# Kernel optimization log

Hardware: AMD Instinct MI355X
Metric: run time of the kernel (lower is better)

Reference implementation:

```python
import jax, jax.numpy as jnp
import numpy as np

UNITS = 512


def setup_inputs() -> dict:
    key = jax.random.key(0)
    k0, k1, k2 = jax.random.split(key, 3)
    batch, timesteps, input_dim = 64, 512, 512
    inputs = jax.random.normal(k0, (batch, timesteps, input_dim), dtype=jnp.float32)
    # Keras glorot_uniform for kernel
    limit = np.sqrt(6.0 / (input_dim + 3 * UNITS))
    kernel = jax.random.uniform(k1, (input_dim, 3 * UNITS), dtype=jnp.float32,
                                minval=-limit, maxval=limit)
    # orthogonal init for recurrent kernel
    recurrent_kernel = jax.nn.initializers.orthogonal()(k2, (UNITS, 3 * UNITS), jnp.float32)
    bias = jnp.zeros((2, 3 * UNITS), dtype=jnp.float32)
    return {"inputs": inputs, "kernel": kernel,
            "recurrent_kernel": recurrent_kernel, "bias": bias}


def _gru_forward(inputs, kernel, recurrent_kernel, bias):
    units = recurrent_kernel.shape[0]
    batch = inputs.shape[0]
    input_bias, recurrent_bias = bias[0], bias[1]
    # Precompute input projections for all timesteps: [B, T, 3U]
    x_all = jnp.einsum('bti,ig->btg', inputs, kernel) + input_bias
    x_all_t = jnp.swapaxes(x_all, 0, 1)  # [T, B, 3U] for scan
    h0 = jnp.zeros((batch, units), dtype=inputs.dtype)

    def step(h, x_t):
        x_z, x_r, x_h = jnp.split(x_t, 3, axis=-1)
        rec = h @ recurrent_kernel + recurrent_bias  # [B, 3U]
        rec_z, rec_r, rec_h = jnp.split(rec, 3, axis=-1)
        z = jax.nn.sigmoid(x_z + rec_z)
        r = jax.nn.sigmoid(x_r + rec_r)
        hh = jnp.tanh(x_h + r * rec_h)
        h_new = z * h + (1.0 - z) * hh
        return h_new, h_new

    _, outs = jax.lax.scan(step, h0, x_all_t)  # outs: [T, B, U]
    return jnp.swapaxes(outs, 0, 1)  # [B, T, U] (return_sequences=True)


def reference(inputs, kernel, recurrent_kernel, bias):
    return _gru_forward(inputs, kernel, recurrent_kernel, bias)
```

## Files before the change

### kernel.cpp

```cpp
#include <hip/hip_runtime.h>
#include <hip/hip_bf16.h>


typedef float f32x4 __attribute__((ext_vector_type(4)));
typedef float f32x2 __attribute__((ext_vector_type(2)));
typedef short bf16x8 __attribute__((ext_vector_type(8)));
typedef unsigned long long u64;
typedef unsigned int u32;
typedef unsigned short u16;
typedef u32 u32x4 __attribute__((ext_vector_type(4)));

#define MFMA16(a, b, c) __builtin_amdgcn_mfma_f32_16x16x32_bf16((a), (b), (c), 0, 0, 0)

__device__ __forceinline__ float bf2f(__hip_bfloat16 v) { return __bfloat162float(v); }

__device__ __forceinline__ void split_bf(float v, short& hi, short& lo) {
    __hip_bfloat16 h = __float2bfloat16(v);
    float rem = v - __bfloat162float(h);
    __hip_bfloat16 l = __float2bfloat16(rem);
    hi = __builtin_bit_cast(short, h);
    lo = __builtin_bit_cast(short, l);
}

__device__ __forceinline__ void wg_barrier() {
    __builtin_amdgcn_sched_barrier(0);
    asm volatile("s_waitcnt lgkmcnt(0)" ::: "memory");
    __builtin_amdgcn_s_barrier();
    __builtin_amdgcn_sched_barrier(0);
}

__global__ void zero_kernel(float* p, int n) {
    int i = blockIdx.x * blockDim.x + threadIdx.x;
    int stride = gridDim.x * blockDim.x;
    for (; i < n; i += stride) p[i] = 0.f;
}

__global__ __launch_bounds__(64, 1) void pack_w_kernel(const float* __restrict__ W,
                                                       short* __restrict__ dhi,
                                                       short* __restrict__ dlo) {
    int bid = blockIdx.x;
    int lane = threadIdx.x;
    int col = (bid >> 4) * 16 + (lane & 15);
    int kbase = (bid & 15) * 32 + (lane >> 4) * 8;
    bf16x8 vh, vl;
#pragma unroll
    for (int e = 0; e < 8; e++) {
        float v = W[(kbase + e) * 1536 + col];
        short h, l;
        split_bf(v, h, l);
        vh[e] = h;
        vl[e] = l;
    }
    *(bf16x8*)(dhi + bid * 512 + lane * 8) = vh;
    *(bf16x8*)(dlo + bid * 512 + lane * 8) = vl;
}

__global__ __launch_bounds__(256, 2) void xgemm_kernel(
    const float* __restrict__ A, const short* __restrict__ wkh,
    const short* __restrict__ wkl, const float* __restrict__ bias,
    __hip_bfloat16* __restrict__ xhi, __hip_bfloat16* __restrict__ xlo, int xlo_en) {
    int rt = blockIdx.x;
    int wave = threadIdx.x >> 6, lane = threadIdx.x & 63;
    int arow = rt * 16 + (lane & 15);
    const float* abase = A + arow * 512 + (lane >> 4) * 8;

    f32x4 acc[24];
#pragma unroll
    for (int j = 0; j < 24; j++) acc[j] = (f32x4){0.f, 0.f, 0.f, 0.f};

#pragma unroll 1
    for (int kk = 0; kk < 16; kk++) {
        f32x4 a0 = *(const f32x4*)(abase + kk * 32);
        f32x4 a1 = *(const f32x4*)(abase + kk * 32 + 4);
        bf16x8 ah, al;
#pragma unroll
        for (int e = 0; e < 8; e++) {
            float v = (e < 4) ? a0[e] : a1[e - 4];
            short h, l;
            split_bf(v, h, l);
            ah[e] = h;
            al[e] = l;
        }
#pragma unroll
        for (int j = 0; j < 24; j++) {
            int frag = (wave * 24 + j) * 16 + kk;
            bf16x8 bh = *(const bf16x8*)(wkh + frag * 512 + lane * 8);
            bf16x8 bl = *(const bf16x8*)(wkl + frag * 512 + lane * 8);
            acc[j] = MFMA16(ah, bh, acc[j]);
            acc[j] = MFMA16(al, bh, acc[j]);
            acc[j] = MFMA16(ah, bl, acc[j]);
        }
    }
    int colin = lane & 15, r4 = (lane >> 4) * 4;
#pragma unroll
    for (int j = 0; j < 24; j++) {
        int colg = (wave * 24 + j) * 16 + colin;
        float bv = bias[colg];
#pragma unroll
        for (int r = 0; r < 4; r++) {
            float v = acc[j][r] + bv;
            int rowg = rt * 16 + r4 + r;
            short h, l;
            split_bf(v, h, l);
            xhi[rowg * 1536 + colg] = __builtin_bit_cast(__hip_bfloat16, h);
            if (xlo_en) xlo[rowg * 1536 + colg] = __builtin_bit_cast(__hip_bfloat16, l);
        }
    }
}

__global__ __launch_bounds__(512, 1) void scan_kernel(
    const __hip_bfloat16* __restrict__ xhi, const __hip_bfloat16* __restrict__ xlo,
    const short* __restrict__ wrh, const short* __restrict__ wrl,
    const float* __restrict__ bias, float* __restrict__ out,
    u64* hbuf2, int xlo_en) {
    const int bid = blockIdx.x;
    const int g = bid & 3;
    const int w = bid >> 2;
    const int tid = threadIdx.x;
    const int wave = tid >> 6;
    const int lane = tid & 63;

    __shared__ __align__(16) float pre[6][16][16];
    __shared__ __align__(16) __hip_bfloat16 xsh[2][2][16][104];
    __shared__ __align__(16) __hip_bfloat16 hsh[2][2][16][512];
    __shared__ float rb[96];

    if (tid < 96) rb[tid] = bias[1536 + (tid >> 5) * 512 + w * 32 + (tid & 31)];

    bf16x8 bh[16], bl[16];
    if (wave < 6) {
        int tile = (wave >> 1) * 32 + 2 * w + (wave & 1);
#pragma unroll
        for (int kk = 0; kk < 16; kk++) {
            bh[kk] = *(const bf16x8*)(wrh + (tile * 16 + kk) * 512 + lane * 8);
            bl[kk] = *(const bf16x8*)(wrl + (tile * 16 + kk) * 512 + lane * 8);
        }
#pragma unroll
        for (int kk = 0; kk < 16; kk++) {
            asm volatile("" : "+v"(bh[kk]), "+v"(bl[kk]));
        }
    } else {
        int it0 = tid - 384;
        int nch = xlo_en ? 384 : 192;
        for (int c = it0; c < nch; c += 128) {
            int plane = c / 192, rem = c % 192;
            int row_ = rem / 12, cw = rem % 12;
            const __hip_bfloat16* src = (plane ? xlo : xhi) +
                                        (size_t)((g * 16 + row_) * 512) * 1536 +
                                        (cw >> 2) * 512 + w * 32 + (cw & 3) * 8;
            *(bf16x8*)&xsh[0][plane][row_][(cw >> 2) * 32 + (cw & 3) * 8] =
                *(const bf16x8*)src;
        }
    }

    const int grow = tid & 15;
    const int q = tid >> 4;
    float h0 = 0.f, h1 = 0.f;
    const int hslot = w * 256 + (grow + 16 * (q >> 2)) * 4 + (q & 3);
    const int sA = tid * 4;
    const int sB = 2048 + tid * 4;
    const int xit = tid - 384;

    u32* hshu = (u32*)hsh;

    __syncthreads();

    for (int t = 0; t < 512; t++) {
        const int par = t & 1;
        u64 sv[8];
        {
            const u64* gb = hbuf2 + ((size_t)(((t - 1) & 1) * 4 + g)) * 4096;
            if (t == 0) {
#pragma unroll
                for (int j = 0; j < 4; j++)
                    sv[j] = __hip_atomic_load(gb + sA + j, __ATOMIC_RELAXED,
                                              __HIP_MEMORY_SCOPE_AGENT);
#pragma unroll
                for (int j = 0; j < 4; j++)
                    sv[4 + j] = __hip_atomic_load(gb + sB + j, __ATOMIC_RELAXED,
                                                  __HIP_MEMORY_SCOPE_AGENT);
            } else {
                const int expv = ((t - 1) % 3) + 1;
                const u64 expm =
                    ((u64)(expv & 1) << 32) | ((u64)((expv >> 1) & 1) << 48);
                const u64 TAGM = (1ULL << 32) | (1ULL << 48);
                long spins = 0;
                while (true) {
#pragma unroll
                    for (int j = 0; j < 4; j++)
                        sv[j] = __hip_atomic_load(gb + sA + j, __ATOMIC_RELAXED,
                                                  __HIP_MEMORY_SCOPE_AGENT);
#pragma unroll
                    for (int j = 0; j < 4; j++)
                        sv[4 + j] = __hip_atomic_load(gb + sB + j, __ATOMIC_RELAXED,
                                                      __HIP_MEMORY_SCOPE_AGENT);
                    u64 diff = 0;
#pragma unroll
                    for (int j = 0; j < 8; j++) diff |= (sv[j] ^ expm) & TAGM;
                    if (diff == 0) break;
                    if (++spins > (1L << 20)) break;
                }
            }
        }
        bf16x8 xv0, xv1, xv2;
        if (wave >= 6 && t + 1 < 512) {
            int c0 = xit, c1 = xit + 128, c2 = xit + 256;
            {
                int plane = c0 / 192, rem = c0 % 192, row_ = rem / 12, cw = rem % 12;
                xv0 = *(const bf16x8*)((plane ? xlo : xhi) +
                                       (size_t)((g * 16 + row_) * 512 + (t + 1)) * 1536 +
                                       (cw >> 2) * 512 + w * 32 + (cw & 3) * 8);
            }
            if (xlo_en || c1 < 192) {
                int plane = c1 / 192, rem = c1 % 192, row_ = rem / 12, cw = rem % 12;
                xv1 = *(const bf16x8*)((plane ? xlo : xhi) +
                                       (size_t)((g * 16 + row_) * 512 + (t + 1)) * 1536 +
                                       (cw >> 2) * 512 + w * 32 + (cw & 3) * 8);
            }
            if (xlo_en) {
                int plane = 1, rem = c2 % 192, row_ = rem / 12, cw = rem % 12;
                xv2 = *(const bf16x8*)((plane ? xlo : xhi) +
                                       (size_t)((g * 16 + row_) * 512 + (t + 1)) * 1536 +
                                       (cw >> 2) * 512 + w * 32 + (cw & 3) * 8);
            }
        }
        {
            u32* hp = hshu + par * 8192;
            u32x4 a0, a1, b0, b1;
#pragma unroll
            for (int j = 0; j < 4; j++) {
                a0[j] = (u32)sv[j];
                b0[j] = (u32)(sv[j] >> 32);
                a1[j] = (u32)sv[4 + j];
                b1[j] = (u32)(sv[4 + j] >> 32);
            }
            *(u32x4*)&hp[sA] = a0;
            *(u32x4*)&hp[sB] = a1;
            *(u32x4*)&hp[4096 + sA] = b0;
            *(u32x4*)&hp[4096 + sB] = b1;
        }
        wg_barrier();
        if (wave < 6) {
            f32x4 aa = (f32x4){0.f, 0.f, 0.f, 0.f};
            f32x4 ab = (f32x4){0.f, 0.f, 0.f, 0.f};
            f32x4 ac = (f32x4){0.f, 0.f, 0.f, 0.f};
#pragma unroll
            for (int kk = 0; kk < 16; kk++) {
                bf16x8 ah = *(const bf16x8*)&hsh[par][0][kk][lane * 8];
                bf16x8 al = *(const bf16x8*)&hsh[par][1][kk][lane * 8];
                aa = MFMA16(ah, bh[kk], aa);
                ab = MFMA16(al, bh[kk], ab);
                ac = MFMA16(ah, bl[kk], ac);
            }
            f32x4 acc = aa + ab;
            acc = acc + ac;
            *(f32x4*)&pre[wave][lane & 15][(lane >> 4) * 4] = acc;
        } else if (t + 1 < 512) {
            int npar = (t + 1) & 1;
            int c0 = xit, c1 = xit + 128, c2 = xit + 256;
            {
                int plane = c0 / 192, rem = c0 % 192, row_ = rem / 12, cw = rem % 12;
                *(bf16x8*)&xsh[npar][plane][row_][(cw >> 2) * 32 + (cw & 3) * 8] = xv0;
            }
            if (xlo_en || c1 < 192) {
                int plane = c1 / 192, rem = c1 % 192, row_ = rem / 12, cw = rem % 12;
                *(bf16x8*)&xsh[npar][plane][row_][(cw >> 2) * 32 + (cw & 3) * 8] = xv1;
            }
            if (xlo_en) {
                int plane = 1, rem = c2 % 192, row_ = rem / 12, cw = rem % 12;
                *(bf16x8*)&xsh[npar][plane][row_][(cw >> 2) * 32 + (cw & 3) * 8] = xv2;
            }
        }
        wg_barrier();
        if (tid < 256) {
            float hold[2] = {h0, h1};
            float hn[2];
#pragma unroll
            for (int j = 0; j < 2; j++) {
                int uu = 2 * q + j;
                int sl = uu >> 4, c16 = uu & 15;
                float xz = bf2f(xsh[par][0][grow][uu]);
                float xr = bf2f(xsh[par][0][grow][32 + uu]);
                float xh = bf2f(xsh[par][0][grow][64 + uu]);
                if (xlo_en) {
                    xz += bf2f(xsh[par][1][grow][uu]);
                    xr += bf2f(xsh[par][1][grow][32 + uu]);
                    xh += bf2f(xsh[par][1][grow][64 + uu]);
                }
                float rz = pre[sl][c16][grow] + rb[uu];
                float rr = pre[2 + sl][c16][grow] + rb[32 + uu];
                float rh = pre[4 + sl][c16][grow] + rb[64 + uu];
                float z = 1.f / (1.f + expf(-(xz + rz)));
                float r = 1.f / (1.f + expf(-(xr + rr)));
                float hh = tanhf(xh + r * rh);
                hn[j] = z * hold[j] + (1.f - z) * hh;
            }
            h0 = hn[0];
            h1 = hn[1];
            if (t < 511) {
                short hi0, lo0, hi1, lo1;
                split_bf(hn[0], hi0, lo0);
                split_bf(hn[1], hi1, lo1);
                const u32 tag = (u32)(t % 3) + 1;
                u32 lo0m = ((u32)(u16)lo0 & ~1u) | (tag & 1);
                u32 lo1m = ((u32)(u16)lo1 & ~1u) | ((tag >> 1) & 1);
                u64 v = (u64)(u16)hi0 | ((u64)(u16)hi1 << 16) | ((u64)lo0m << 32) |
                        ((u64)lo1m << 48);
                __hip_atomic_store(&hbuf2[((size_t)(par * 4 + g)) * 4096 + hslot], v,
                                   __ATOMIC_RELAXED, __HIP_MEMORY_SCOPE_AGENT);
            }
            *(f32x2*)&out[((size_t)(g * 16 + grow) * 512 + t) * 512 + w * 32 + 2 * q] =
                (f32x2){h0, h1};
        }
    }
}

extern "C" void kernel_launch(void* const* d_in, const int* in_sizes, int n_in,
                              void* d_out, int out_size, void* d_ws, size_t ws_size,
                              hipStream_t stream) {
    const float* inputs = (const float*)d_in[0];
    const float* wk = (const float*)d_in[1];
    const float* wr = (const float*)d_in[2];
    const float* bias = (const float*)d_in[3];
    float* out = (float*)d_out;
    char* ws = (char*)d_ws;

    const size_t SZ_W = 512UL * 1536 * 2;
    short* wk_hi = (short*)(ws);
    short* wk_lo = (short*)(ws + SZ_W);
    short* wr_hi = (short*)(ws + 2 * SZ_W);
    short* wr_lo = (short*)(ws + 3 * SZ_W);
    u64* hbuf2 = (u64*)(ws + 4 * SZ_W);
    char* xbase = ws + 4 * SZ_W + 262144;
    const size_t SZ_X = 32768UL * 1536 * 2;
    __hip_bfloat16* xhi = (__hip_bfloat16*)xbase;
    __hip_bfloat16* xlo = (__hip_bfloat16*)(xbase + SZ_X);

    size_t need_min = (size_t)(xbase - ws) + SZ_X;
    size_t need_full = need_min + SZ_X;
    if (ws_size < need_min) return;
    int xlo_en = (ws_size >= need_full) ? 1 : 0;

    zero_kernel<<<256, 256, 0, stream>>>((float*)hbuf2, 262144 / 4);
    pack_w_kernel<<<1536, 64, 0, stream>>>(wk, wk_hi, wk_lo);
    pack_w_kernel<<<1536, 64, 0, stream>>>(wr, wr_hi, wr_lo);
    xgemm_kernel<<<2048, 256, 0, stream>>>(inputs, wk_hi, wk_lo, bias, xhi, xlo, xlo_en);
    scan_kernel<<<64, 512, 0, stream>>>(xhi, xlo, wr_hi, wr_lo, bias, out, hbuf2,
                                        xlo_en);
}
```

Measured before the change: 2.521 ms.

## Retile input GEMM into row-pair by column-group blocks and move h polling to waves 4-7

The input-projection GEMM now gives each block two 16-row tiles and one third of the output columns, launched over 3072 blocks. Each loaded weight fragment is reused across both row tiles and fewer accumulators are held per wave. In the scan kernel, only the four non-MFMA waves (4-7) poll the global hidden-state buffer and copy it into LDS. The MFMA waves go straight to the barrier, and the x prefetch stores are issued after the barrier to overlap with the recurrent MFMA. This is meant to shorten the per-step critical path, at the cost of more loads per polling thread and a changed barrier pattern.

```diff
diff --git a/kernel.cpp b/kernel.cpp
--- a/kernel.cpp
+++ b/kernel.cpp
@@ -59,51 +59,70 @@
     const float* __restrict__ A, const short* __restrict__ wkh,
     const short* __restrict__ wkl, const float* __restrict__ bias,
     __hip_bfloat16* __restrict__ xhi, __hip_bfloat16* __restrict__ xlo, int xlo_en) {
-    int rt = blockIdx.x;
+    int bid = blockIdx.x;
+    int cg = bid % 3;
+    int rp = bid / 3;
     int wave = threadIdx.x >> 6, lane = threadIdx.x & 63;
-    int arow = rt * 16 + (lane & 15);
-    const float* abase = A + arow * 512 + (lane >> 4) * 8;
-
-    f32x4 acc[24];
-#pragma unroll
-    for (int j = 0; j < 24; j++) acc[j] = (f32x4){0.f, 0.f, 0.f, 0.f};
+    int arow0 = rp * 32 + (lane & 15);
+    const float* ab0 = A + (size_t)arow0 * 512 + (lane >> 4) * 8;
+    const float* ab1 = ab0 + 16 * 512;
+
+    f32x4 acc[2][8];
+#pragma unroll
+    for (int r = 0; r < 2; r++)
+#pragma unroll
+        for (int j = 0; j < 8; j++) acc[r][j] = (f32x4){0.f, 0.f, 0.f, 0.f};
 
 #pragma unroll 1
     for (int kk = 0; kk < 16; kk++) {
-        f32x4 a0 = *(const f32x4*)(abase + kk * 32);
-        f32x4 a1 = *(const f32x4*)(abase + kk * 32 + 4);
-        bf16x8 ah, al;
+        f32x4 a00 = *(const f32x4*)(ab0 + kk * 32);
+        f32x4 a01 = *(const f32x4*)(ab0 + kk * 32 + 4);
+        f32x4 a10 = *(const f32x4*)(ab1 + kk * 32);
+        f32x4 a11 = *(const f32x4*)(ab1 + kk * 32 + 4);
+        bf16x8 ah0, al0, ah1, al1;
 #pragma unroll
         for (int e = 0; e < 8; e++) {
-            float v = (e < 4) ? a0[e] : a1[e - 4];
+            float v0 = (e < 4) ? a00[e] : a01[e - 4];
+            float v1 = (e < 4) ? a10[e] : a11[e - 4];
             short h, l;
-            split_bf(v, h, l);
-            ah[e] = h;
-            al[e] = l;
-        }
-#pragma unroll
-        for (int j = 0; j < 24; j++) {
-            int frag = (wave * 24 + j) * 16 + kk;
+            split_bf(v0, h, l);
+            ah0[e] = h;
+            al0[e] = l;
+            split_bf(v1, h, l);
+            ah1[e] = h;
+            al1[e] = l;
+        }
+#pragma unroll
+        for (int j = 0; j < 8; j++) {
+            int frag = (cg * 32 + wave * 8 + j) * 16 + kk;
             bf16x8 bh = *(const bf16x8*)(wkh + frag * 512 + lane * 8);
             bf16x8 bl = *(const bf16x8*)(wkl + frag * 512 + lane * 8);
-            acc[j] = MFMA16(ah, bh, acc[j]);
-            acc[j] = MFMA16(al, bh, acc[j]);
-            acc[j] = MFMA16(ah, bl, acc[j]);
+            acc[0][j] = MFMA16(ah0, bh, acc[0][j]);
+            acc[0][j] = MFMA16(al0, bh, acc[0][j]);
+            acc[0][j] = MFMA16(ah0, bl, acc[0][j]);
+            acc[1][j] = MFMA16(ah1, bh, acc[1][j]);
+            acc[1][j] = MFMA16(al1, bh, acc[1][j]);
+            acc[1][j] = MFMA16(ah1, bl, acc[1][j]);
         }
     }
     int colin = lane & 15, r4 = (lane >> 4) * 4;
 #pragma unroll
-    for (int j = 0; j < 24; j++) {
-        int colg = (wave * 24 + j) * 16 + colin;
+    for (int j = 0; j < 8; j++) {
+        int colg = (cg * 32 + wave * 8 + j) * 16 + colin;
         float bv = bias[colg];
 #pragma unroll
-        for (int r = 0; r < 4; r++) {
-            float v = acc[j][r] + bv;
-            int rowg = rt * 16 + r4 + r;
-            short h, l;
-            split_bf(v, h, l);
-            xhi[rowg * 1536 + colg] = __builtin_bit_cast(__hip_bfloat16, h);
-            if (xlo_en) xlo[rowg * 1536 + colg] = __builtin_bit_cast(__hip_bfloat16, l);
+        for (int rt = 0; rt < 2; rt++) {
+#pragma unroll
+            for (int r = 0; r < 4; r++) {
+                float v = acc[rt][j][r] + bv;
+                int rowg = rp * 32 + rt * 16 + r4 + r;
+                short h, l;
+                split_bf(v, h, l);
+                xhi[(size_t)rowg * 1536 + colg] = __builtin_bit_cast(__hip_bfloat16, h);
+                if (xlo_en)
+                    xlo[(size_t)rowg * 1536 + colg] =
+                        __builtin_bit_cast(__hip_bfloat16, l);
+            }
         }
     }
 }
@@ -139,7 +158,8 @@
         for (int kk = 0; kk < 16; kk++) {
             asm volatile("" : "+v"(bh[kk]), "+v"(bl[kk]));
         }
-    } else {
+    }
+    if (wave >= 6) {
         int it0 = tid - 384;
         int nch = xlo_en ? 384 : 192;
         for (int c = it0; c < nch; c += 128) {
@@ -157,8 +177,7 @@
     const int q = tid >> 4;
     float h0 = 0.f, h1 = 0.f;
     const int hslot = w * 256 + (grow + 16 * (q >> 2)) * 4 + (q & 3);
-    const int sA = tid * 4;
-    const int sB = 2048 + tid * 4;
+    const int st = tid - 256;
     const int xit = tid - 384;
 
     u32* hshu = (u32*)hsh;
@@ -167,79 +186,110 @@
 
     for (int t = 0; t < 512; t++) {
         const int par = t & 1;
-        u64 sv[8];
-        {
-            const u64* gb = hbuf2 + ((size_t)(((t - 1) & 1) * 4 + g)) * 4096;
-            if (t == 0) {
-#pragma unroll
-                for (int j = 0; j < 4; j++)
-                    sv[j] = __hip_atomic_load(gb + sA + j, __ATOMIC_RELAXED,
-                                              __HIP_MEMORY_SCOPE_AGENT);
-#pragma unroll
-                for (int j = 0; j < 4; j++)
-                    sv[4 + j] = __hip_atomic_load(gb + sB + j, __ATOMIC_RELAXED,
+        if (wave >= 4) {
+            bf16x8 xv0, xv1, xv2;
+            if (wave >= 6 && t + 1 < 512) {
+                int c0 = xit, c1 = xit + 128, c2 = xit + 256;
+                {
+                    int plane = c0 / 192, rem = c0 % 192, row_ = rem / 12,
+                        cw = rem % 12;
+                    xv0 = *(const bf16x8*)((plane ? xlo : xhi) +
+                                           (size_t)((g * 16 + row_) * 512 + (t + 1)) *
+                                               1536 +
+                                           (cw >> 2) * 512 + w * 32 + (cw & 3) * 8);
+                }
+                if (xlo_en || c1 < 192) {
+                    int plane = c1 / 192, rem = c1 % 192, row_ = rem / 12,
+                        cw = rem % 12;
+                    xv1 = *(const bf16x8*)((plane ? xlo : xhi) +
+                                           (size_t)((g * 16 + row_) * 512 + (t + 1)) *
+                                               1536 +
+                                           (cw >> 2) * 512 + w * 32 + (cw & 3) * 8);
+                }
+                if (xlo_en) {
+                    int plane = 1, rem = c2 % 192, row_ = rem / 12, cw = rem % 12;
+                    xv2 = *(const bf16x8*)((plane ? xlo : xhi) +
+                                           (size_t)((g * 16 + row_) * 512 + (t + 1)) *
+                                               1536 +
+                                           (cw >> 2) * 512 + w * 32 + (cw & 3) * 8);
+                }
+            }
+            u64 sv[16];
+            {
+                const u64* gb = hbuf2 + ((size_t)(((t - 1) & 1) * 4 + g)) * 4096;
+                if (t == 0) {
+#pragma unroll
+                    for (int r = 0; r < 4; r++)
+#pragma unroll
+                        for (int j = 0; j < 4; j++)
+                            sv[r * 4 + j] =
+                                __hip_atomic_load(gb + r * 1024 + st * 4 + j,
+                                                  __ATOMIC_RELAXED,
                                                   __HIP_MEMORY_SCOPE_AGENT);
+                } else {
+                    const int expv = ((t - 1) % 3) + 1;
+                    const u64 expm =
+                        ((u64)(expv & 1) << 32) | ((u64)((expv >> 1) & 1) << 48);
+                    const u64 TAGM = (1ULL << 32) | (1ULL << 48);
+                    long spins = 0;
+                    while (true) {
+#pragma unroll
+                        for (int r = 0; r < 4; r++)
+#pragma unroll
+                            for (int j = 0; j < 4; j++)
+                                sv[r * 4 + j] =
+                                    __hip_atomic_load(gb + r * 1024 + st * 4 + j,
+                                                      __ATOMIC_RELAXED,
+                                                      __HIP_MEMORY_SCOPE_AGENT);
+                        u64 diff = 0;
+#pragma unroll
+                        for (int k = 0; k < 16; k++) diff |= (sv[k] ^ expm) & TAGM;
+                        if (diff == 0) break;
+                        if (++spins > (1L << 20)) break;
+                    }
+                }
+            }
+            {
+                u32* hp = hshu + par * 8192;
+#pragma unroll
+                for (int r = 0; r < 4; r++) {
+                    u32x4 vlo, vhi;
+#pragma unroll
+                    for (int j = 0; j < 4; j++) {
+                        vlo[j] = (u32)sv[r * 4 + j];
+                        vhi[j] = (u32)(sv[r * 4 + j] >> 32);
+                    }
+                    *(u32x4*)&hp[r * 1024 + st * 4] = vlo;
+                    *(u32x4*)&hp[4096 + r * 1024 + st * 4] = vhi;
+                }
+            }
+            if (wave >= 6 && t + 1 < 512) {
+                wg_barrier();
+                int npar = (t + 1) & 1;
+                int c0 = xit, c1 = xit + 128, c2 = xit + 256;
+                {
+                    int plane = c0 / 192, rem = c0 % 192, row_ = rem / 12,
+                        cw = rem % 12;
+                    *(bf16x8*)&xsh[npar][plane][row_][(cw >> 2) * 32 + (cw & 3) * 8] =
+                        xv0;
+                }
+                if (xlo_en || c1 < 192) {
+                    int plane = c1 / 192, rem = c1 % 192, row_ = rem / 12,
+                        cw = rem % 12;
+                    *(bf16x8*)&xsh[npar][plane][row_][(cw >> 2) * 32 + (cw & 3) * 8] =
+                        xv1;
+                }
+                if (xlo_en) {
+                    int plane = 1, rem = c2 % 192, row_ = rem / 12, cw = rem % 12;
+                    *(bf16x8*)&xsh[npar][plane][row_][(cw >> 2) * 32 + (cw & 3) * 8] =
+                        xv2;
+                }
             } else {
-                const int expv = ((t - 1) % 3) + 1;
-                const u64 expm =
-                    ((u64)(expv & 1) << 32) | ((u64)((expv >> 1) & 1) << 48);
-                const u64 TAGM = (1ULL << 32) | (1ULL << 48);
-                long spins = 0;
-                while (true) {
-#pragma unroll
-                    for (int j = 0; j < 4; j++)
-                        sv[j] = __hip_atomic_load(gb + sA + j, __ATOMIC_RELAXED,
-                                                  __HIP_MEMORY_SCOPE_AGENT);
-#pragma unroll
-                    for (int j = 0; j < 4; j++)
-                        sv[4 + j] = __hip_atomic_load(gb + sB + j, __ATOMIC_RELAXED,
-                                                      __HIP_MEMORY_SCOPE_AGENT);
-                    u64 diff = 0;
-#pragma unroll
-                    for (int j = 0; j < 8; j++) diff |= (sv[j] ^ expm) & TAGM;
-                    if (diff == 0) break;
-                    if (++spins > (1L << 20)) break;
-                }
-            }
-        }
-        bf16x8 xv0, xv1, xv2;
-        if (wave >= 6 && t + 1 < 512) {
-            int c0 = xit, c1 = xit + 128, c2 = xit + 256;
-            {
-                int plane = c0 / 192, rem = c0 % 192, row_ = rem / 12, cw = rem % 12;
-                xv0 = *(const bf16x8*)((plane ? xlo : xhi) +
-                                       (size_t)((g * 16 + row_) * 512 + (t + 1)) * 1536 +
-                                       (cw >> 2) * 512 + w * 32 + (cw & 3) * 8);
-            }
-            if (xlo_en || c1 < 192) {
-                int plane = c1 / 192, rem = c1 % 192, row_ = rem / 12, cw = rem % 12;
-                xv1 = *(const bf16x8*)((plane ? xlo : xhi) +
-                                       (size_t)((g * 16 + row_) * 512 + (t + 1)) * 1536 +
-                                       (cw >> 2) * 512 + w * 32 + (cw & 3) * 8);
-            }
-            if (xlo_en) {
-                int plane = 1, rem = c2 % 192, row_ = rem / 12, cw = rem % 12;
-                xv2 = *(const bf16x8*)((plane ? xlo : xhi) +
-                                       (size_t)((g * 16 + row_) * 512 + (t + 1)) * 1536 +
-                                       (cw >> 2) * 512 + w * 32 + (cw & 3) * 8);
-            }
-        }
-        {
-            u32* hp = hshu + par * 8192;
-            u32x4 a0, a1, b0, b1;
-#pragma unroll
-            for (int j = 0; j < 4; j++) {
-                a0[j] = (u32)sv[j];
-                b0[j] = (u32)(sv[j] >> 32);
-                a1[j] = (u32)sv[4 + j];
-                b1[j] = (u32)(sv[4 + j] >> 32);
-            }
-            *(u32x4*)&hp[sA] = a0;
-            *(u32x4*)&hp[sB] = a1;
-            *(u32x4*)&hp[4096 + sA] = b0;
-            *(u32x4*)&hp[4096 + sB] = b1;
-        }
-        wg_barrier();
+                wg_barrier();
+            }
+        } else {
+            wg_barrier();
+        }
         if (wave < 6) {
             f32x4 aa = (f32x4){0.f, 0.f, 0.f, 0.f};
             f32x4 ab = (f32x4){0.f, 0.f, 0.f, 0.f};
@@ -255,21 +305,6 @@
             f32x4 acc = aa + ab;
             acc = acc + ac;
             *(f32x4*)&pre[wave][lane & 15][(lane >> 4) * 4] = acc;
-        } else if (t + 1 < 512) {
-            int npar = (t + 1) & 1;
-            int c0 = xit, c1 = xit + 128, c2 = xit + 256;
-            {
-                int plane = c0 / 192, rem = c0 % 192, row_ = rem / 12, cw = rem % 12;
-                *(bf16x8*)&xsh[npar][plane][row_][(cw >> 2) * 32 + (cw & 3) * 8] = xv0;
-            }
-            if (xlo_en || c1 < 192) {
-                int plane = c1 / 192, rem = c1 % 192, row_ = rem / 12, cw = rem % 12;
-                *(bf16x8*)&xsh[npar][plane][row_][(cw >> 2) * 32 + (cw & 3) * 8] = xv1;
-            }
-            if (xlo_en) {
-                int plane = 1, rem = c2 % 192, row_ = rem / 12, cw = rem % 12;
-                *(bf16x8*)&xsh[npar][plane][row_][(cw >> 2) * 32 + (cw & 3) * 8] = xv2;
-            }
         }
         wg_barrier();
         if (tid < 256) {
@@ -344,7 +379,7 @@
     zero_kernel<<<256, 256, 0, stream>>>((float*)hbuf2, 262144 / 4);
     pack_w_kernel<<<1536, 64, 0, stream>>>(wk, wk_hi, wk_lo);
     pack_w_kernel<<<1536, 64, 0, stream>>>(wr, wr_hi, wr_lo);
-    xgemm_kernel<<<2048, 256, 0, stream>>>(inputs, wk_hi, wk_lo, bias, xhi, xlo, xlo_en);
+    xgemm_kernel<<<3072, 256, 0, stream>>>(inputs, wk_hi, wk_lo, bias, xhi, xlo, xlo_en);
     scan_kernel<<<64, 512, 0, stream>>>(xhi, xlo, wr_hi, wr_lo, bias, out, hbuf2,
                                         xlo_en);
 }
```

After: 2.555 ms. About the same (+1.4%).

## Retile input GEMM for weight reuse and double-buffer scan spin-wait loads

Applied to the files above, without the earlier changes.

The input projection GEMM now has each block compute a 64-row by 512-column tile using 512 threads. Each weight fragment load is reused across four row tiles, where before every 16-row block streamed the entire weight matrix, so global weight traffic drops. In the scan, the polling loop alternates between two register buffers, so the next load is already in flight while the previous result's tags are checked, which shortens the latency of cross-block hidden-state handoffs. The cost is more register pressure in the GEMM from 16 accumulators plus the A fragments, and extra registers in the scan loop.

```diff
diff --git a/kernel.cpp b/kernel.cpp
--- a/kernel.cpp
+++ b/kernel.cpp
@@ -55,55 +55,70 @@
     *(bf16x8*)(dlo + bid * 512 + lane * 8) = vl;
 }
 
-__global__ __launch_bounds__(256, 2) void xgemm_kernel(
+__global__ __launch_bounds__(512, 1) void xgemm_kernel(
     const float* __restrict__ A, const short* __restrict__ wkh,
     const short* __restrict__ wkl, const float* __restrict__ bias,
     __hip_bfloat16* __restrict__ xhi, __hip_bfloat16* __restrict__ xlo, int xlo_en) {
-    int rt = blockIdx.x;
+    int bid = blockIdx.x;
+    int cg = bid % 3;
+    int rb = bid / 3;
     int wave = threadIdx.x >> 6, lane = threadIdx.x & 63;
-    int arow = rt * 16 + (lane & 15);
-    const float* abase = A + arow * 512 + (lane >> 4) * 8;
-
-    f32x4 acc[24];
-#pragma unroll
-    for (int j = 0; j < 24; j++) acc[j] = (f32x4){0.f, 0.f, 0.f, 0.f};
+    int arow0 = rb * 64 + (lane & 15);
+    const float* ab = A + (size_t)arow0 * 512 + (lane >> 4) * 8;
+
+    f32x4 acc[4][4];
+#pragma unroll
+    for (int rt = 0; rt < 4; rt++)
+#pragma unroll
+        for (int j = 0; j < 4; j++) acc[rt][j] = (f32x4){0.f, 0.f, 0.f, 0.f};
 
 #pragma unroll 1
     for (int kk = 0; kk < 16; kk++) {
-        f32x4 a0 = *(const f32x4*)(abase + kk * 32);
-        f32x4 a1 = *(const f32x4*)(abase + kk * 32 + 4);
-        bf16x8 ah, al;
-#pragma unroll
-        for (int e = 0; e < 8; e++) {
-            float v = (e < 4) ? a0[e] : a1[e - 4];
-            short h, l;
-            split_bf(v, h, l);
-            ah[e] = h;
-            al[e] = l;
-        }
-#pragma unroll
-        for (int j = 0; j < 24; j++) {
-            int frag = (wave * 24 + j) * 16 + kk;
-            bf16x8 bh = *(const bf16x8*)(wkh + frag * 512 + lane * 8);
-            bf16x8 bl = *(const bf16x8*)(wkl + frag * 512 + lane * 8);
-            acc[j] = MFMA16(ah, bh, acc[j]);
-            acc[j] = MFMA16(al, bh, acc[j]);
-            acc[j] = MFMA16(ah, bl, acc[j]);
+        bf16x8 ah[4], al[4];
+#pragma unroll
+        for (int rt = 0; rt < 4; rt++) {
+            f32x4 a0 = *(const f32x4*)(ab + (size_t)rt * 16 * 512 + kk * 32);
+            f32x4 a1 = *(const f32x4*)(ab + (size_t)rt * 16 * 512 + kk * 32 + 4);
+#pragma unroll
+            for (int e = 0; e < 8; e++) {
+                float v = (e < 4) ? a0[e] : a1[e - 4];
+                short h, l;
+                split_bf(v, h, l);
+                ah[rt][e] = h;
+                al[rt][e] = l;
+            }
+        }
+#pragma unroll
+        for (int j = 0; j < 4; j++) {
+            int frag = (cg * 32 + wave * 4 + j) * 16 + kk;
+            bf16x8 bh = *(const bf16x8*)(wkh + (size_t)frag * 512 + lane * 8);
+            bf16x8 bl = *(const bf16x8*)(wkl + (size_t)frag * 512 + lane * 8);
+#pragma unroll
+            for (int rt = 0; rt < 4; rt++) {
+                acc[rt][j] = MFMA16(ah[rt], bh, acc[rt][j]);
+                acc[rt][j] = MFMA16(al[rt], bh, acc[rt][j]);
+                acc[rt][j] = MFMA16(ah[rt], bl, acc[rt][j]);
+            }
         }
     }
     int colin = lane & 15, r4 = (lane >> 4) * 4;
 #pragma unroll
-    for (int j = 0; j < 24; j++) {
-        int colg = (wave * 24 + j) * 16 + colin;
+    for (int j = 0; j < 4; j++) {
+        int colg = (cg * 32 + wave * 4 + j) * 16 + colin;
         float bv = bias[colg];
 #pragma unroll
-        for (int r = 0; r < 4; r++) {
-            float v = acc[j][r] + bv;
-            int rowg = rt * 16 + r4 + r;
-            short h, l;
-            split_bf(v, h, l);
-            xhi[rowg * 1536 + colg] = __builtin_bit_cast(__hip_bfloat16, h);
-            if (xlo_en) xlo[rowg * 1536 + colg] = __builtin_bit_cast(__hip_bfloat16, l);
+        for (int rt = 0; rt < 4; rt++) {
+#pragma unroll
+            for (int r = 0; r < 4; r++) {
+                float v = acc[rt][j][r] + bv;
+                int rowg = rb * 64 + rt * 16 + r4 + r;
+                short h, l;
+                split_bf(v, h, l);
+                xhi[(size_t)rowg * 1536 + colg] = __builtin_bit_cast(__hip_bfloat16, h);
+                if (xlo_en)
+                    xlo[(size_t)rowg * 1536 + colg] =
+                        __builtin_bit_cast(__hip_bfloat16, l);
+            }
         }
     }
 }
@@ -167,41 +182,70 @@
 
     for (int t = 0; t < 512; t++) {
         const int par = t & 1;
-        u64 sv[8];
-        {
-            const u64* gb = hbuf2 + ((size_t)(((t - 1) & 1) * 4 + g)) * 4096;
-            if (t == 0) {
-#pragma unroll
-                for (int j = 0; j < 4; j++)
-                    sv[j] = __hip_atomic_load(gb + sA + j, __ATOMIC_RELAXED,
-                                              __HIP_MEMORY_SCOPE_AGENT);
-#pragma unroll
-                for (int j = 0; j < 4; j++)
-                    sv[4 + j] = __hip_atomic_load(gb + sB + j, __ATOMIC_RELAXED,
-                                                  __HIP_MEMORY_SCOPE_AGENT);
-            } else {
-                const int expv = ((t - 1) % 3) + 1;
-                const u64 expm =
-                    ((u64)(expv & 1) << 32) | ((u64)((expv >> 1) & 1) << 48);
-                const u64 TAGM = (1ULL << 32) | (1ULL << 48);
-                long spins = 0;
-                while (true) {
-#pragma unroll
-                    for (int j = 0; j < 4; j++)
-                        sv[j] = __hip_atomic_load(gb + sA + j, __ATOMIC_RELAXED,
-                                                  __HIP_MEMORY_SCOPE_AGENT);
-#pragma unroll
-                    for (int j = 0; j < 4; j++)
-                        sv[4 + j] = __hip_atomic_load(gb + sB + j, __ATOMIC_RELAXED,
-                                                      __HIP_MEMORY_SCOPE_AGENT);
+        const u64* gb = hbuf2 + ((size_t)(((t - 1) & 1) * 4 + g)) * 4096;
+
+        u32* hp = hshu + par * 8192;
+        auto unpack8 = [&](const u64* sv) __attribute__((always_inline)) {
+            u32x4 a0, a1, b0, b1;
+#pragma unroll
+            for (int j = 0; j < 4; j++) {
+                a0[j] = (u32)sv[j];
+                b0[j] = (u32)(sv[j] >> 32);
+                a1[j] = (u32)sv[4 + j];
+                b1[j] = (u32)(sv[4 + j] >> 32);
+            }
+            *(u32x4*)&hp[sA] = a0;
+            *(u32x4*)&hp[sB] = a1;
+            *(u32x4*)&hp[4096 + sA] = b0;
+            *(u32x4*)&hp[4096 + sB] = b1;
+        };
+
+        u64 sva[8], svb[8];
+#define LOAD8(dst)                                                                   \
+    do {                                                                             \
+        _Pragma("unroll") for (int j = 0; j < 4; j++) dst[j] =                       \
+            __hip_atomic_load(gb + sA + j, __ATOMIC_RELAXED,                         \
+                              __HIP_MEMORY_SCOPE_AGENT);                             \
+        _Pragma("unroll") for (int j = 0; j < 4; j++) dst[4 + j] =                   \
+            __hip_atomic_load(gb + sB + j, __ATOMIC_RELAXED,                         \
+                              __HIP_MEMORY_SCOPE_AGENT);                             \
+    } while (0)
+
+        if (t == 0) {
+            LOAD8(sva);
+            unpack8(sva);
+        } else {
+            const int expv = ((t - 1) % 3) + 1;
+            const u64 expm = ((u64)(expv & 1) << 32) | ((u64)((expv >> 1) & 1) << 48);
+            const u64 TAGM = (1ULL << 32) | (1ULL << 48);
+            LOAD8(sva);
+            long spins = 0;
+            int winner = 0;
+            while (true) {
+                if (winner == 0) {
+                    LOAD8(svb);
                     u64 diff = 0;
 #pragma unroll
-                    for (int j = 0; j < 8; j++) diff |= (sv[j] ^ expm) & TAGM;
+                    for (int j = 0; j < 8; j++) diff |= (sva[j] ^ expm) & TAGM;
                     if (diff == 0) break;
-                    if (++spins > (1L << 20)) break;
+                    winner = 1;
+                } else {
+                    LOAD8(sva);
+                    u64 diff = 0;
+#pragma unroll
+                    for (int j = 0; j < 8; j++) diff |= (svb[j] ^ expm) & TAGM;
+                    if (diff == 0) break;
+                    winner = 0;
                 }
-            }
-        }
+                if (++spins > (1L << 20)) break;
+            }
+            if (winner == 0)
+                unpack8(sva);
+            else
+                unpack8(svb);
+        }
+#undef LOAD8
+
         bf16x8 xv0, xv1, xv2;
         if (wave >= 6 && t + 1 < 512) {
             int c0 = xit, c1 = xit + 128, c2 = xit + 256;
@@ -223,21 +267,6 @@
                                        (size_t)((g * 16 + row_) * 512 + (t + 1)) * 1536 +
                                        (cw >> 2) * 512 + w * 32 + (cw & 3) * 8);
             }
-        }
-        {
-            u32* hp = hshu + par * 8192;
-            u32x4 a0, a1, b0, b1;
-#pragma unroll
-            for (int j = 0; j < 4; j++) {
-                a0[j] = (u32)sv[j];
-                b0[j] = (u32)(sv[j] >> 32);
-                a1[j] = (u32)sv[4 + j];
-                b1[j] = (u32)(sv[4 + j] >> 32);
-            }
-            *(u32x4*)&hp[sA] = a0;
-            *(u32x4*)&hp[sB] = a1;
-            *(u32x4*)&hp[4096 + sA] = b0;
-            *(u32x4*)&hp[4096 + sB] = b1;
         }
         wg_barrier();
         if (wave < 6) {
@@ -344,7 +373,7 @@
     zero_kernel<<<256, 256, 0, stream>>>((float*)hbuf2, 262144 / 4);
     pack_w_kernel<<<1536, 64, 0, stream>>>(wk, wk_hi, wk_lo);
     pack_w_kernel<<<1536, 64, 0, stream>>>(wr, wr_hi, wr_lo);
-    xgemm_kernel<<<2048, 256, 0, stream>>>(inputs, wk_hi, wk_lo, bias, xhi, xlo, xlo_en);
+    xgemm_kernel<<<1536, 512, 0, stream>>>(inputs, wk_hi, wk_lo, bias, xhi, xlo, xlo_en);
     scan_kernel<<<64, 512, 0, stream>>>(xhi, xlo, wr_hi, wr_lo, bias, out, hbuf2,
                                         xlo_en);
 }
```

New measurement: 2.808 ms. +11.4%, slower.
